# Kernel optimization log

Measured on AMD Instinct MI355X. Metric: run time of the kernel, lower is better.

## Reference

```python
import jax, jax.numpy as jnp
import numpy as np

V, E, H, S, B, MAX_OOV = 50000, 256, 512, 500, 64, 50


def setup_inputs() -> dict:
    key = jax.random.key(0)
    ks = jax.random.split(key, 22)
    s = 0.02  # param init scale
    return {
        "input_token": jax.random.randint(ks[0], (B, 1), 0, V),
        "encoder_hidden_states": jax.random.normal(ks[1], (S, B, 2 * H), jnp.float32),
        "projected_encoder_hidden_states": jax.random.normal(ks[2], (S, B, H), jnp.float32),
        "src_mask": jnp.ones((B, S), dtype=bool),
        "prev_hidden": jax.random.normal(ks[3], (1, B, H), jnp.float32),
        "encoder_batch_extended_vocab": jax.random.randint(ks[4], (B, S), 0, V + MAX_OOV),
        "batch_max_oov": MAX_OOV,
        # learned parameters
        "emb": jax.random.normal(ks[5], (V, E), jnp.float32) * s,
        "attn_Wq": jax.random.normal(ks[6], (H, H), jnp.float32) * s,   # query_layer, no bias
        "attn_We": jax.random.normal(ks[7], (1, H), jnp.float32) * s,   # energy_layer, no bias
        "gru_Wih": jax.random.normal(ks[8], (3 * H, E + 2 * H), jnp.float32) * s,
        "gru_Whh": jax.random.normal(ks[9], (3 * H, H), jnp.float32) * s,
        "gru_bih": jax.random.normal(ks[10], (3 * H,), jnp.float32) * s,
        "gru_bhh": jax.random.normal(ks[11], (3 * H,), jnp.float32) * s,
        "lin_W": jax.random.normal(ks[12], (H, E + 3 * H), jnp.float32) * s,
        "lin_b": jax.random.normal(ks[13], (H,), jnp.float32) * s,
        "pg_W": jax.random.normal(ks[14], (1, E + 3 * H), jnp.float32) * s,
        "pg_b": jax.random.normal(ks[15], (1,), jnp.float32) * s,
        "out_W": jax.random.normal(ks[16], (V, H), jnp.float32) * s,
        "out_b": jax.random.normal(ks[17], (V,), jnp.float32) * s,
    }


def _forward(input_token, enc_h, proj_key, prev_hidden, ext_vocab, max_oov,
             emb, attn_Wq, attn_We, gru_Wih, gru_Whh, gru_bih, gru_bhh,
             lin_W, lin_b, pg_W, pg_b, out_W, out_b):
    b = input_token.shape[0]
    embed = jnp.transpose(emb[input_token], (1, 0, 2))  # [1,B,E]

    # Bahdanau attention (softmax over source dim 0; mask unused, as in source)
    q = jnp.einsum('tbh,oh->tbo', prev_hidden, attn_Wq)            # [1,B,H]
    scores = jnp.einsum('sbh,oh->sb', jnp.tanh(q + proj_key), attn_We)  # [S,B]
    alphas = jax.nn.softmax(scores, axis=0)                        # [S,B]
    context = jnp.einsum('sb,sbd->bd', alphas, enc_h)[None]        # [1,B,2H]
    attention_dist = alphas.T                                      # [B,S]

    # GRU cell (torch gate order: r, z, n)
    x = jnp.concatenate([embed, context], axis=2)[0]               # [B,E+2H]
    h = prev_hidden[0]                                             # [B,H]
    gi = x @ gru_Wih.T + gru_bih                                   # [B,3H]
    gh = h @ gru_Whh.T + gru_bhh
    i_r, i_z, i_n = jnp.split(gi, 3, axis=1)
    h_r, h_z, h_n = jnp.split(gh, 3, axis=1)
    r = jax.nn.sigmoid(i_r + h_r)
    z = jax.nn.sigmoid(i_z + h_z)
    n = jnp.tanh(i_n + r * h_n)
    h_new = (1.0 - z) * n + z * h                                  # [B,H]
    rnn_output = h_new[None]                                       # [1,B,H]

    concat = jnp.concatenate([embed, rnn_output, context], axis=2)  # [1,B,E+3H]
    p_gen = jax.nn.sigmoid(jnp.einsum('tbf,of->tbo', concat, pg_W) + pg_b)  # [1,B,1]
    lin = jnp.einsum('tbf,of->tbo', concat, lin_W) + lin_b          # [1,B,H]
    logits = jnp.einsum('tbh,vh->tbv', lin, out_W) + out_b          # [1,B,V]

    gen_prob = p_gen * jax.nn.softmax(logits, axis=2)               # [1,B,V]
    attn_prob = ((1.0 - p_gen) * attention_dist[None])[0]           # [B,S]

    ext = jnp.concatenate(
        [gen_prob, jnp.zeros((1, b, max_oov), gen_prob.dtype)], axis=2) + 1e-12  # [1,B,V+oov]
    rows = jnp.arange(b)[:, None]
    merged = ext.at[0, rows, ext_vocab].add(attn_prob)              # scatter_add over vocab dim
    output = jnp.log(merged)
    return output, h_new[None]


def reference(input_token, encoder_hidden_states, projected_encoder_hidden_states,
              src_mask, prev_hidden, encoder_batch_extended_vocab, batch_max_oov,
              emb, attn_Wq, attn_We, gru_Wih, gru_Whh, gru_bih, gru_bhh,
              lin_W, lin_b, pg_W, pg_b, out_W, out_b):
    return _forward(input_token, encoder_hidden_states, projected_encoder_hidden_states,
                    prev_hidden, encoder_batch_extended_vocab, batch_max_oov,
                    emb, attn_Wq, attn_We, gru_Wih, gru_Whh, gru_bih, gru_bhh,
                    lin_W, lin_b, pg_W, pg_b, out_W, out_b)
```

## Files before the change

### kernel.cpp

```cpp
#include <hip/hip_runtime.h>
#include <hip/hip_bf16.h>
#include <math.h>

namespace {
constexpr int V = 50000, E = 256, H = 512, S = 500, B = 64, OOVN = 50;
constexpr int VEXT = V + OOVN;
constexpr int CCAT = E + 3 * H;
constexpr int G3 = 3 * H;
constexpr int NLB = 391;

typedef __attribute__((ext_vector_type(8))) short short8;
typedef __attribute__((ext_vector_type(4))) float f32x4;

__device__ __forceinline__ float wsum(float v) {
#pragma unroll
  for (int off = 32; off > 0; off >>= 1) v += __shfl_xor(v, off, 64);
  return v;
}
__device__ __forceinline__ float sigmoidf(float x) { return 1.f / (1.f + __expf(-x)); }
__device__ __forceinline__ float fast_tanh(float x) {
  x = fminf(fmaxf(x, -15.f), 15.f);
  float e = __expf(2.f * x);
  return __fdividef(e - 1.f, e + 1.f);
}
__device__ __forceinline__ void smerge_s(float& m, float& l, float om, float ol) {
  float nm = fmaxf(m, om);
  if (nm == -INFINITY) { m = nm; return; }
  l = l * __expf(m - nm) + ol * __expf(om - nm);
  m = nm;
}
__device__ __forceinline__ short bf16_rn_s(float f) {
  __hip_bfloat16 h = __float2bfloat16(f);
  return __builtin_bit_cast(short, h);
}
__device__ __forceinline__ float bf16s_to_f(unsigned short u) {
  return __uint_as_float(((unsigned)u) << 16);
}
__device__ __forceinline__ void hilo8(float4 a, float4 b, short8& hi, short8& lo) {
  float f[8] = {a.x, a.y, a.z, a.w, b.x, b.y, b.z, b.w};
#pragma unroll
  for (int i = 0; i < 8; ++i) {
    unsigned u = __float_as_uint(f[i]);
    hi[i] = (short)(u >> 16);
    lo[i] = bf16_rn_s(f[i] - __uint_as_float(u & 0xffff0000u));
  }
}

template <int KSTEPS>
__device__ __forceinline__ void gemm_core_f32(const float* __restrict__ X, int ldx,
                                              int xk0, const float* __restrict__ W,
                                              int ldw, int wk0, int n0, f32x4 acc[4]) {
  const int l = threadIdx.x & 63;
  const int r16 = l & 15, q16 = l >> 4;
#pragma unroll
  for (int t = 0; t < 4; ++t) acc[t] = (f32x4){0.f, 0.f, 0.f, 0.f};
  const float* wp = W + (size_t)(n0 + r16) * ldw + wk0 + q16 * 8;
  const float* xp[4];
#pragma unroll
  for (int t = 0; t < 4; ++t) xp[t] = X + (size_t)(t * 16 + r16) * ldx + xk0 + q16 * 8;
#pragma unroll
  for (int ks = 0; ks < KSTEPS; ++ks) {
    const int ko = ks * 32;
    float4 w0 = *reinterpret_cast<const float4*>(wp + ko);
    float4 w1 = *reinterpret_cast<const float4*>(wp + ko + 4);
    short8 whi, wlo;
    hilo8(w0, w1, whi, wlo);
#pragma unroll
    for (int t = 0; t < 4; ++t) {
      float4 x0 = *reinterpret_cast<const float4*>(xp[t] + ko);
      float4 x1 = *reinterpret_cast<const float4*>(xp[t] + ko + 4);
      short8 ah, al;
      hilo8(x0, x1, ah, al);
      acc[t] = __builtin_amdgcn_mfma_f32_16x16x32_bf16(ah, whi, acc[t], 0, 0, 0);
      acc[t] = __builtin_amdgcn_mfma_f32_16x16x32_bf16(al, whi, acc[t], 0, 0, 0);
      acc[t] = __builtin_amdgcn_mfma_f32_16x16x32_bf16(ah, wlo, acc[t], 0, 0, 0);
    }
  }
}
template <int KSTEPS>
__device__ __forceinline__ void gemm_store_f32(const float* X, int ldx, int xk0,
                                               const float* W, int ldw, int wk0, int n0,
                                               float* C, int ldc) {
  f32x4 acc[4];
  gemm_core_f32<KSTEPS>(X, ldx, xk0, W, ldw, wk0, n0, acc);
  const int l = threadIdx.x & 63;
  const int r16 = l & 15, q16 = l >> 4;
#pragma unroll
  for (int t = 0; t < 4; ++t)
#pragma unroll
    for (int r = 0; r < 4; ++r) {
      int row = t * 16 + q16 * 4 + r;
      C[(size_t)row * ldc + n0 + r16] = acc[t][r];
    }
}

__global__ void __launch_bounds__(256) k_head(const float* __restrict__ prevh,
                                              const float* __restrict__ Wq,
                                              const float* __restrict__ Whh,
                                              const int* __restrict__ tok,
                                              const float* __restrict__ emb,
                                              float* __restrict__ qpart,
                                              float* __restrict__ ghp,
                                              float* __restrict__ cc) {
  int gw = blockIdx.x * 4 + (threadIdx.x >> 6);
  if (gw < 128) {
    int c = gw >> 5, nt = gw & 31;
    gemm_store_f32<4>(prevh, H, c * 128, Wq, H, c * 128, nt * 16,
                      qpart + (size_t)c * 64 * H, H);
  } else if (gw < 320) {
    int w2 = gw - 128;
    int c = w2 / 96, nt = w2 % 96;
    gemm_store_f32<8>(prevh, H, c * 256, Whh, H, c * 256, nt * 16,
                      ghp + (size_t)c * 64 * G3, G3);
  } else {
    int idx = (gw - 320) * 64 + (threadIdx.x & 63);
    for (int i = idx; i < B * E; i += 1024) {
      int b = i >> 8, e = i & 255;
      cc[b * CCAT + e] = emb[(size_t)tok[b] * E + e];
    }
  }
}

__global__ void __launch_bounds__(256) k_attn(
    const float* __restrict__ qpart, const float* __restrict__ pk,
    const float* __restrict__ We, const float* __restrict__ ench,
    float* __restrict__ scoresT, float* __restrict__ ctxp, float* __restrict__ pml) {
  int x = blockIdx.x;
  int b = x >> 5, ch = x & 31;
  int s0 = ch * 16;
  int cnt = (ch == 31) ? 4 : 16;
  int t = threadIdx.x, w = t >> 6, lane = t & 63;
  __shared__ float es[16];
  float4 q0 = {0.f, 0.f, 0.f, 0.f}, q1 = {0.f, 0.f, 0.f, 0.f};
#pragma unroll
  for (int c = 0; c < 4; ++c) {
    const float* qb = qpart + ((size_t)c * 64 + b) * H + lane * 8;
    float4 a0 = *reinterpret_cast<const float4*>(qb);
    float4 a1 = *reinterpret_cast<const float4*>(qb + 4);
    q0.x += a0.x; q0.y += a0.y; q0.z += a0.z; q0.w += a0.w;
    q1.x += a1.x; q1.y += a1.y; q1.z += a1.z; q1.w += a1.w;
  }
  float4 e0 = *reinterpret_cast<const float4*>(We + lane * 8);
  float4 e1 = *reinterpret_cast<const float4*>(We + lane * 8 + 4);
  for (int j = w; j < cnt; j += 4) {
    int s = s0 + j;
    const float* kr = pk + ((size_t)s * B + b) * H + lane * 8;
    float4 k0 = *reinterpret_cast<const float4*>(kr);
    float4 k1 = *reinterpret_cast<const float4*>(kr + 4);
    float part = fast_tanh(q0.x + k0.x) * e0.x + fast_tanh(q0.y + k0.y) * e0.y +
                 fast_tanh(q0.z + k0.z) * e0.z + fast_tanh(q0.w + k0.w) * e0.w +
                 fast_tanh(q1.x + k1.x) * e1.x + fast_tanh(q1.y + k1.y) * e1.y +
                 fast_tanh(q1.z + k1.z) * e1.z + fast_tanh(q1.w + k1.w) * e1.w;
    part = wsum(part);
    if (lane == 0) { es[j] = part; scoresT[b * S + s] = part; }
  }
  __syncthreads();
  if (w == 0) {
    float v = (lane < cnt) ? es[lane] : -INFINITY;
    float m = v;
#pragma unroll
    for (int off = 32; off > 0; off >>= 1) m = fmaxf(m, __shfl_xor(m, off, 64));
    float e = (lane < cnt) ? __expf(v - m) : 0.f;
    float l = wsum(e);
    if (lane < cnt) es[lane] = e;
    if (lane == 0) { pml[2 * x] = m; pml[2 * x + 1] = l; }
  }
  __syncthreads();
  float4 acc = {0.f, 0.f, 0.f, 0.f};
  const float* eb = ench + ((size_t)s0 * B + b) * 1024 + t * 4;
#pragma unroll
  for (int j = 0; j < 16; ++j) {
    if (j < cnt) {
      float wgt = es[j];
      float4 v = *reinterpret_cast<const float4*>(eb + (size_t)j * (B * 1024));
      acc.x += wgt * v.x; acc.y += wgt * v.y; acc.z += wgt * v.z; acc.w += wgt * v.w;
    }
  }
  *reinterpret_cast<float4*>(ctxp + (size_t)x * 1024 + t * 4) = acc;
}

__global__ void __launch_bounds__(256) k_attn2(
    const float* __restrict__ ctxp, const float* __restrict__ pml,
    const float* __restrict__ scoresT, float* __restrict__ cc,
    float* __restrict__ alphasT) {
  int b = blockIdx.x, t = threadIdx.x;
  float m = -INFINITY;
#pragma unroll
  for (int ch = 0; ch < 32; ++ch) m = fmaxf(m, pml[2 * (b * 32 + ch)]);
  float L = 0.f;
  float sc[32];
#pragma unroll
  for (int ch = 0; ch < 32; ++ch) {
    float sf = __expf(pml[2 * (b * 32 + ch)] - m);
    sc[ch] = sf;
    L += pml[2 * (b * 32 + ch) + 1] * sf;
  }
  float inv = 1.f / L;
  float4 acc = {0.f, 0.f, 0.f, 0.f};
#pragma unroll
  for (int ch = 0; ch < 32; ++ch) {
    float4 v = *reinterpret_cast<const float4*>(ctxp + (size_t)(b * 32 + ch) * 1024 + t * 4);
    acc.x += sc[ch] * v.x; acc.y += sc[ch] * v.y;
    acc.z += sc[ch] * v.z; acc.w += sc[ch] * v.w;
  }
  acc.x *= inv; acc.y *= inv; acc.z *= inv; acc.w *= inv;
  *reinterpret_cast<float4*>(cc + b * CCAT + 768 + t * 4) = acc;
  for (int s = t; s < S; s += 256)
    alphasT[b * S + s] = __expf(scoresT[b * S + s] - m) * inv;
}

__global__ void __launch_bounds__(256) k_gemm_big(const float* __restrict__ cc,
                                                  const float* __restrict__ Wih,
                                                  const float* __restrict__ linW,
                                                  float* __restrict__ gip,
                                                  float* __restrict__ linpart) {
  int w = blockIdx.x * 4 + (threadIdx.x >> 6);
  if (w < 480) {
    int c = w / 96, nt = w % 96;
    int xk0 = (c == 0) ? 0 : 768 + (c - 1) * 256;
    gemm_store_f32<8>(cc, CCAT, xk0, Wih, 1280, c * 256, nt * 16,
                      gip + (size_t)c * 64 * G3, G3);
  } else {
    int w2 = w - 480;
    int c = w2 >> 5, nt = w2 & 31;
    int k0 = (c == 0) ? 0 : 768 + (c - 1) * 256;
    gemm_store_f32<8>(cc, CCAT, k0, linW, CCAT, k0, nt * 16,
                      linpart + (size_t)c * 64 * H, H);
  }
}

__global__ void k_gates(const float* __restrict__ gip, const float* __restrict__ ghp,
                        const float* __restrict__ bih, const float* __restrict__ bhh,
                        const float* __restrict__ prevh, const float* __restrict__ pgW,
                        const float* __restrict__ pgb, float* __restrict__ cc,
                        float* __restrict__ hout, float* __restrict__ pgsum) {
  int b = blockIdx.x, j = threadIdx.x;
  float ir = bih[j], iz = bih[512 + j], in_ = bih[1024 + j];
#pragma unroll
  for (int c = 0; c < 5; ++c) {
    const float* g = gip + (size_t)c * 64 * G3 + b * G3;
    ir += g[j]; iz += g[512 + j]; in_ += g[1024 + j];
  }
  float hr = bhh[j], hz = bhh[512 + j], hn = bhh[1024 + j];
#pragma unroll
  for (int c = 0; c < 2; ++c) {
    const float* g = ghp + (size_t)c * 64 * G3 + b * G3;
    hr += g[j]; hz += g[512 + j]; hn += g[1024 + j];
  }
  float r = sigmoidf(ir + hr);
  float z = sigmoidf(iz + hz);
  float n = fast_tanh(in_ + r * hn);
  float h = prevh[b * H + j];
  float hnew = (1.f - z) * n + z * h;
  hout[b * H + j] = hnew;
  cc[b * CCAT + E + j] = hnew;
  float acc = hnew * pgW[E + j];
  acc += cc[b * CCAT + 768 + j] * pgW[768 + j];
  acc += cc[b * CCAT + 1280 + j] * pgW[1280 + j];
  if (j < 256) acc += cc[b * CCAT + j] * pgW[j];
  acc = wsum(acc);
  __shared__ float sl[8];
  int w = j >> 6, lane = j & 63;
  if (lane == 0) sl[w] = acc;
  __syncthreads();
  if (j == 0) {
    float tot = pgb[0];
#pragma unroll
    for (int i = 0; i < 8; ++i) tot += sl[i];
    pgsum[b] = tot;
  }
}

__global__ void __launch_bounds__(256) k_linfin(const float* __restrict__ cc,
                                                const float* __restrict__ linW,
                                                const float* __restrict__ linpart,
                                                const float* __restrict__ linb,
                                                short* __restrict__ lh) {
  int w = blockIdx.x * 4 + (threadIdx.x >> 6);
  f32x4 acc[4];
  gemm_core_f32<16>(cc, CCAT, 256, linW, CCAT, 256, w * 16, acc);
  const int l = threadIdx.x & 63;
  const int r16 = l & 15, q16 = l >> 4;
  int col = w * 16 + r16;
  float bv = linb[col];
#pragma unroll
  for (int t = 0; t < 4; ++t)
#pragma unroll
    for (int r = 0; r < 4; ++r) {
      int row = t * 16 + q16 * 4 + r;
      float v = acc[t][r] + bv;
#pragma unroll
      for (int c = 0; c < 5; ++c) v += linpart[(size_t)c * 64 * H + row * H + col];
      lh[row * H + col] = bf16_rn_s(v);
    }
}

__global__ void __launch_bounds__(512) k_gemm_logits(
    const short* __restrict__ lh, const float* __restrict__ outW,
    const float* __restrict__ outb, unsigned short* __restrict__ logitsb,
    float* __restrict__ pm, float* __restrict__ pl) {
  __shared__ __align__(16) short xs[64 * 512];
  __shared__ float pml[8][64][2];
  char* xb = reinterpret_cast<char*>(xs);
  int tid = threadIdx.x;
#pragma unroll
  for (int k = 0; k < 8; ++k) {
    int m = k * 512 + tid;
    int row = m >> 6;
    short8 v = *reinterpret_cast<const short8*>(lh + (size_t)m * 8);
    int byte = (m * 16) ^ ((row & 7) << 4);
    *reinterpret_cast<short8*>(xb + byte) = v;
  }
  __syncthreads();
  const int l = tid & 63;
  const int r16 = l & 15, q16 = l >> 4;
  const int wid = tid >> 6;
  const int waveId = blockIdx.x * 8 + wid;
  const bool active = waveId < V / 16;
  if (active) {
    const int n0 = waveId * 16;
    f32x4 acc[4];
#pragma unroll
    for (int t = 0; t < 4; ++t) acc[t] = (f32x4){0.f, 0.f, 0.f, 0.f};
    const float* wp = outW + (size_t)(n0 + r16) * H + q16 * 8;
    int arow[4], aswz[4];
#pragma unroll
    for (int t = 0; t < 4; ++t) {
      int row = t * 16 + r16;
      arow[t] = row * 1024 + q16 * 16;
      aswz[t] = (row & 7) << 4;
    }
#pragma unroll
    for (int ks = 0; ks < 16; ++ks) {
      float4 w0 = *reinterpret_cast<const float4*>(wp + ks * 32);
      float4 w1 = *reinterpret_cast<const float4*>(wp + ks * 32 + 4);
      short8 wh;
      wh[0] = bf16_rn_s(w0.x); wh[1] = bf16_rn_s(w0.y);
      wh[2] = bf16_rn_s(w0.z); wh[3] = bf16_rn_s(w0.w);
      wh[4] = bf16_rn_s(w1.x); wh[5] = bf16_rn_s(w1.y);
      wh[6] = bf16_rn_s(w1.z); wh[7] = bf16_rn_s(w1.w);
#pragma unroll
      for (int t = 0; t < 4; ++t) {
        short8 a = *reinterpret_cast<const short8*>(xb + ((arow[t] + ks * 64) ^ aswz[t]));
        acc[t] = __builtin_amdgcn_mfma_f32_16x16x32_bf16(a, wh, acc[t], 0, 0, 0);
      }
    }
    float bv = outb[n0 + r16];
#pragma unroll
    for (int t = 0; t < 4; ++t)
#pragma unroll
      for (int r = 0; r < 4; ++r) {
        float y = acc[t][r] + bv;
        int row = t * 16 + q16 * 4 + r;
        logitsb[(size_t)row * V + n0 + r16] = (unsigned short)bf16_rn_s(y);
        float m = y;
#pragma unroll
        for (int off = 8; off > 0; off >>= 1) m = fmaxf(m, __shfl_xor(m, off, 64));
        float e = __expf(y - m);
#pragma unroll
        for (int off = 8; off > 0; off >>= 1) e += __shfl_xor(e, off, 64);
        if (r16 == 0) { pml[wid][row][0] = m; pml[wid][row][1] = e; }
      }
  } else if (r16 == 0) {
#pragma unroll
    for (int t = 0; t < 4; ++t)
#pragma unroll
      for (int r = 0; r < 4; ++r) {
        int row = t * 16 + q16 * 4 + r;
        pml[wid][row][0] = -INFINITY;
        pml[wid][row][1] = 0.f;
      }
  }
  __syncthreads();
  if (tid < 64) {
    float m = pml[0][tid][0], lv = pml[0][tid][1];
#pragma unroll
    for (int i = 1; i < 8; ++i) smerge_s(m, lv, pml[i][tid][0], pml[i][tid][1]);
    pm[blockIdx.x * 64 + tid] = m;
    pl[blockIdx.x * 64 + tid] = lv;
  }
}

__global__ void k_final(const unsigned short* __restrict__ logitsb,
                        const float* __restrict__ pm, const float* __restrict__ pl,
                        const float* __restrict__ pgsum, const int* __restrict__ extv,
                        const float* __restrict__ alphasT, float* __restrict__ out) {
  int b = blockIdx.x, c = blockIdx.y, t = threadIdx.x;
  __shared__ float sp_[5056];
  __shared__ float rm[4], rl[4];
  float m = -INFINITY, lv = 0.f;
  for (int i = t; i < NLB; i += 256) smerge_s(m, lv, pm[i * 64 + b], pl[i * 64 + b]);
#pragma unroll
  for (int off = 32; off > 0; off >>= 1) {
    float om = __shfl_xor(m, off, 64), ol = __shfl_xor(lv, off, 64);
    smerge_s(m, lv, om, ol);
  }
  int w = t >> 6, lane = t & 63;
  if (lane == 0) { rm[w] = m; rl[w] = lv; }
  __syncthreads();
  m = rm[0]; lv = rl[0];
#pragma unroll
  for (int i = 1; i < 4; ++i) smerge_s(m, lv, rm[i], rl[i]);
  float pg = sigmoidf(pgsum[b]);
  float scale = pg / lv;
  const int base = c * 5000;
  const int len = (c == 9) ? 5050 : 5000;
  const unsigned short* lr = logitsb + (size_t)b * V + base;
  for (int i = t; i < len; i += 256)
    sp_[i] = (i < 5000) ? scale * __expf(bf16s_to_f(lr[i]) - m) + 1e-12f : 1e-12f;
  __syncthreads();
  float wgt = 1.f - pg;
  for (int s = t; s < S; s += 256) {
    int idx = extv[b * S + s] - base;
    if ((unsigned)idx < (unsigned)len) atomicAdd(&sp_[idx], wgt * alphasT[b * S + s]);
  }
  __syncthreads();
  float* orow = out + (size_t)b * VEXT + base;
  for (int i = t; i < len; i += 256) orow[i] = __logf(sp_[i]);
}
}

extern "C" void kernel_launch(void* const* d_in, const int* in_sizes, int n_in,
                              void* d_out, int out_size, void* d_ws, size_t ws_size,
                              hipStream_t stream) {
  const int*   tok   = (const int*)d_in[0];
  const float* ench  = (const float*)d_in[1];
  const float* pk    = (const float*)d_in[2];
  const float* prevh = (const float*)d_in[4];
  const int*   extv  = (const int*)d_in[5];
  const float* emb   = (const float*)d_in[7];
  const float* Wq    = (const float*)d_in[8];
  const float* We    = (const float*)d_in[9];
  const float* Wih   = (const float*)d_in[10];
  const float* Whh   = (const float*)d_in[11];
  const float* bih   = (const float*)d_in[12];
  const float* bhh   = (const float*)d_in[13];
  const float* linW  = (const float*)d_in[14];
  const float* linb  = (const float*)d_in[15];
  const float* pgW   = (const float*)d_in[16];
  const float* pgb   = (const float*)d_in[17];
  const float* outW  = (const float*)d_in[18];
  const float* outb  = (const float*)d_in[19];

  float* out = (float*)d_out;
  float* ws = (float*)d_ws;

  float* qpart   = ws;
  float* scoresT = qpart + 131072;
  float* alphasT = scoresT + 32000;
  float* ctxp    = alphasT + 32000;
  float* pml     = ctxp + 2097152;
  float* cc      = pml + 4096;
  float* gip     = cc + 114688;
  float* ghp     = gip + 491520;
  float* linpart = ghp + 196608;
  float* pgsum   = linpart + 163840;
  float* pm      = pgsum + 64;
  float* pl      = pm + 25024;
  unsigned short* logitsb = (unsigned short*)(pl + 25024);
  short* lh      = (short*)(logitsb + (size_t)B * V);
  float* hout    = out + (size_t)B * VEXT;

  k_head<<<dim3(84), dim3(256), 0, stream>>>(prevh, Wq, Whh, tok, emb, qpart, ghp, cc);
  k_attn<<<dim3(2048), dim3(256), 0, stream>>>(qpart, pk, We, ench, scoresT, ctxp, pml);
  k_attn2<<<dim3(B), dim3(256), 0, stream>>>(ctxp, pml, scoresT, cc, alphasT);
  k_gemm_big<<<dim3(160), dim3(256), 0, stream>>>(cc, Wih, linW, gip, linpart);
  k_gates<<<dim3(B), dim3(512), 0, stream>>>(gip, ghp, bih, bhh, prevh, pgW, pgb, cc,
                                             hout, pgsum);
  k_linfin<<<dim3(8), dim3(256), 0, stream>>>(cc, linW, linpart, linb, lh);
  k_gemm_logits<<<dim3(NLB), dim3(512), 0, stream>>>(lh, outW, outb, logitsb, pm, pl);
  k_final<<<dim3(B, 10), dim3(256), 0, stream>>>(logitsb, pm, pl, pgsum, extv, alphasT, out);
}
```

Baseline: 147.4 us.

## Restructure attention kernel to process 4 batches x 8 sources per block

Each attention block now covers 4 batch rows and 8 source positions with 512 threads instead of one batch row and 16 sources with 256 threads, giving 63 source chunks. All key loads are issued up front before the tanh reductions to raise memory-level parallelism, and the context accumulation uses 8-wide vectors per thread. The partial context buffer doubles in size, so the second pass merges 63 chunks per batch and reads twice as much partial data.

Measured after the change: 162.0 us. 9.9% more time.

```diff
diff --git a/kernel.cpp b/kernel.cpp
--- a/kernel.cpp
+++ b/kernel.cpp
@@ -8,6 +8,7 @@
 constexpr int CCAT = E + 3 * H;
 constexpr int G3 = 3 * H;
 constexpr int NLB = 391;
+constexpr int NCH = 63;
 
 typedef __attribute__((ext_vector_type(8))) short short8;
 typedef __attribute__((ext_vector_type(4))) float f32x4;
@@ -121,62 +122,81 @@
   }
 }
 
-__global__ void __launch_bounds__(256) k_attn(
+__global__ void __launch_bounds__(512, 4) k_attn(
     const float* __restrict__ qpart, const float* __restrict__ pk,
     const float* __restrict__ We, const float* __restrict__ ench,
     float* __restrict__ scoresT, float* __restrict__ ctxp, float* __restrict__ pml) {
   int x = blockIdx.x;
-  int b = x >> 5, ch = x & 31;
-  int s0 = ch * 16;
-  int cnt = (ch == 31) ? 4 : 16;
+  int ch = x >> 4, bg = x & 15;
+  int b0 = bg * 4;
+  int s0 = ch * 8;
+  int cnt = (ch == NCH - 1) ? 4 : 8;
   int t = threadIdx.x, w = t >> 6, lane = t & 63;
-  __shared__ float es[16];
-  float4 q0 = {0.f, 0.f, 0.f, 0.f}, q1 = {0.f, 0.f, 0.f, 0.f};
+  __shared__ float es[8][4];
+  int bl1 = w & 3, sh = w >> 2;
+  f32x4 qa = {0.f, 0.f, 0.f, 0.f}, qb_ = {0.f, 0.f, 0.f, 0.f};
 #pragma unroll
   for (int c = 0; c < 4; ++c) {
-    const float* qb = qpart + ((size_t)c * 64 + b) * H + lane * 8;
-    float4 a0 = *reinterpret_cast<const float4*>(qb);
-    float4 a1 = *reinterpret_cast<const float4*>(qb + 4);
-    q0.x += a0.x; q0.y += a0.y; q0.z += a0.z; q0.w += a0.w;
-    q1.x += a1.x; q1.y += a1.y; q1.z += a1.z; q1.w += a1.w;
-  }
-  float4 e0 = *reinterpret_cast<const float4*>(We + lane * 8);
-  float4 e1 = *reinterpret_cast<const float4*>(We + lane * 8 + 4);
-  for (int j = w; j < cnt; j += 4) {
-    int s = s0 + j;
-    const float* kr = pk + ((size_t)s * B + b) * H + lane * 8;
-    float4 k0 = *reinterpret_cast<const float4*>(kr);
-    float4 k1 = *reinterpret_cast<const float4*>(kr + 4);
-    float part = fast_tanh(q0.x + k0.x) * e0.x + fast_tanh(q0.y + k0.y) * e0.y +
-                 fast_tanh(q0.z + k0.z) * e0.z + fast_tanh(q0.w + k0.w) * e0.w +
-                 fast_tanh(q1.x + k1.x) * e1.x + fast_tanh(q1.y + k1.y) * e1.y +
-                 fast_tanh(q1.z + k1.z) * e1.z + fast_tanh(q1.w + k1.w) * e1.w;
+    const float* qb = qpart + ((size_t)c * 64 + b0 + bl1) * H + lane * 8;
+    qa += *reinterpret_cast<const f32x4*>(qb);
+    qb_ += *reinterpret_cast<const f32x4*>(qb + 4);
+  }
+  f32x4 e0 = *reinterpret_cast<const f32x4*>(We + lane * 8);
+  f32x4 e1 = *reinterpret_cast<const f32x4*>(We + lane * 8 + 4);
+  f32x4 ka[4], kb[4];
+#pragma unroll
+  for (int j = 0; j < 4; ++j) {
+    int s_l = sh * 4 + j;
+    int s = s0 + ((s_l < cnt) ? s_l : cnt - 1);
+    const float* kr = pk + ((size_t)s * B + b0 + bl1) * H + lane * 8;
+    ka[j] = *reinterpret_cast<const f32x4*>(kr);
+    kb[j] = *reinterpret_cast<const f32x4*>(kr + 4);
+  }
+#pragma unroll
+  for (int j = 0; j < 4; ++j) {
+    int s_l = sh * 4 + j;
+    float part = fast_tanh(qa[0] + ka[j][0]) * e0[0] + fast_tanh(qa[1] + ka[j][1]) * e0[1] +
+                 fast_tanh(qa[2] + ka[j][2]) * e0[2] + fast_tanh(qa[3] + ka[j][3]) * e0[3] +
+                 fast_tanh(qb_[0] + kb[j][0]) * e1[0] + fast_tanh(qb_[1] + kb[j][1]) * e1[1] +
+                 fast_tanh(qb_[2] + kb[j][2]) * e1[2] + fast_tanh(qb_[3] + kb[j][3]) * e1[3];
     part = wsum(part);
-    if (lane == 0) { es[j] = part; scoresT[b * S + s] = part; }
-  }
-  __syncthreads();
-  if (w == 0) {
-    float v = (lane < cnt) ? es[lane] : -INFINITY;
+    if (lane == 0 && s_l < cnt) {
+      es[s_l][bl1] = part;
+      scoresT[(b0 + bl1) * S + s0 + s_l] = part;
+    }
+  }
+  __syncthreads();
+  if (w < 4) {
+    float v = (lane < cnt) ? es[lane][w] : -INFINITY;
     float m = v;
 #pragma unroll
     for (int off = 32; off > 0; off >>= 1) m = fmaxf(m, __shfl_xor(m, off, 64));
     float e = (lane < cnt) ? __expf(v - m) : 0.f;
     float l = wsum(e);
-    if (lane < cnt) es[lane] = e;
-    if (lane == 0) { pml[2 * x] = m; pml[2 * x + 1] = l; }
-  }
-  __syncthreads();
-  float4 acc = {0.f, 0.f, 0.f, 0.f};
-  const float* eb = ench + ((size_t)s0 * B + b) * 1024 + t * 4;
-#pragma unroll
-  for (int j = 0; j < 16; ++j) {
-    if (j < cnt) {
-      float wgt = es[j];
-      float4 v = *reinterpret_cast<const float4*>(eb + (size_t)j * (B * 1024));
-      acc.x += wgt * v.x; acc.y += wgt * v.y; acc.z += wgt * v.z; acc.w += wgt * v.w;
-    }
-  }
-  *reinterpret_cast<float4*>(ctxp + (size_t)x * 1024 + t * 4) = acc;
+    if (lane < 8) es[lane][w] = (lane < cnt) ? e : 0.f;
+    if (lane == 0) {
+      pml[2 * (ch * 64 + b0 + w)] = m;
+      pml[2 * (ch * 64 + b0 + w) + 1] = l;
+    }
+  }
+  __syncthreads();
+  int bl3 = t >> 7, d8 = (t & 127) * 8;
+  float wg[8];
+#pragma unroll
+  for (int j = 0; j < 8; ++j) wg[j] = es[j][bl3];
+  f32x4 acc0 = {0.f, 0.f, 0.f, 0.f}, acc1 = {0.f, 0.f, 0.f, 0.f};
+#pragma unroll
+  for (int j = 0; j < 8; ++j) {
+    int jc = (j < cnt) ? j : cnt - 1;
+    const float* er = ench + ((size_t)(s0 + jc) * B + b0 + bl3) * 1024 + d8;
+    f32x4 v0 = *reinterpret_cast<const f32x4*>(er);
+    f32x4 v1 = *reinterpret_cast<const f32x4*>(er + 4);
+    acc0 += wg[j] * v0;
+    acc1 += wg[j] * v1;
+  }
+  float* cp = ctxp + ((size_t)x * 4 + bl3) * 1024 + d8;
+  *reinterpret_cast<f32x4*>(cp) = acc0;
+  *reinterpret_cast<f32x4*>(cp + 4) = acc1;
 }
 
 __global__ void __launch_bounds__(256) k_attn2(
@@ -184,25 +204,19 @@
     const float* __restrict__ scoresT, float* __restrict__ cc,
     float* __restrict__ alphasT) {
   int b = blockIdx.x, t = threadIdx.x;
+  int bg = b >> 2, bl = b & 3;
   float m = -INFINITY;
-#pragma unroll
-  for (int ch = 0; ch < 32; ++ch) m = fmaxf(m, pml[2 * (b * 32 + ch)]);
+  for (int ch = 0; ch < NCH; ++ch) m = fmaxf(m, pml[2 * (ch * 64 + b)]);
   float L = 0.f;
-  float sc[32];
-#pragma unroll
-  for (int ch = 0; ch < 32; ++ch) {
-    float sf = __expf(pml[2 * (b * 32 + ch)] - m);
-    sc[ch] = sf;
-    L += pml[2 * (b * 32 + ch) + 1] * sf;
+  float4 acc = {0.f, 0.f, 0.f, 0.f};
+  for (int ch = 0; ch < NCH; ++ch) {
+    float sf = __expf(pml[2 * (ch * 64 + b)] - m);
+    L += pml[2 * (ch * 64 + b) + 1] * sf;
+    float4 v = *reinterpret_cast<const float4*>(
+        ctxp + ((size_t)(ch * 16 + bg) * 4 + bl) * 1024 + t * 4);
+    acc.x += sf * v.x; acc.y += sf * v.y; acc.z += sf * v.z; acc.w += sf * v.w;
   }
   float inv = 1.f / L;
-  float4 acc = {0.f, 0.f, 0.f, 0.f};
-#pragma unroll
-  for (int ch = 0; ch < 32; ++ch) {
-    float4 v = *reinterpret_cast<const float4*>(ctxp + (size_t)(b * 32 + ch) * 1024 + t * 4);
-    acc.x += sc[ch] * v.x; acc.y += sc[ch] * v.y;
-    acc.z += sc[ch] * v.z; acc.w += sc[ch] * v.w;
-  }
   acc.x *= inv; acc.y *= inv; acc.z *= inv; acc.w *= inv;
   *reinterpret_cast<float4*>(cc + b * CCAT + 768 + t * 4) = acc;
   for (int s = t; s < S; s += 256)
@@ -449,8 +463,8 @@
   float* scoresT = qpart + 131072;
   float* alphasT = scoresT + 32000;
   float* ctxp    = alphasT + 32000;
-  float* pml     = ctxp + 2097152;
-  float* cc      = pml + 4096;
+  float* pml     = ctxp + 4128768;
+  float* cc      = pml + 8192;
   float* gip     = cc + 114688;
   float* ghp     = gip + 491520;
   float* linpart = ghp + 196608;
@@ -462,7 +476,7 @@
   float* hout    = out + (size_t)B * VEXT;
 
   k_head<<<dim3(84), dim3(256), 0, stream>>>(prevh, Wq, Whh, tok, emb, qpart, ghp, cc);
-  k_attn<<<dim3(2048), dim3(256), 0, stream>>>(qpart, pk, We, ench, scoresT, ctxp, pml);
+  k_attn<<<dim3(NCH * 16), dim3(512), 0, stream>>>(qpart, pk, We, ench, scoresT, ctxp, pml);
   k_attn2<<<dim3(B), dim3(256), 0, stream>>>(ctxp, pml, scoresT, cc, alphasT);
   k_gemm_big<<<dim3(160), dim3(256), 0, stream>>>(cc, Wih, linW, gip, linpart);
   k_gates<<<dim3(B), dim3(512), 0, stream>>>(gip, ghp, bih, bhh, prevh, pgW, pgb, cc,
```
